# Kernel tuning notes

Hardware: AMD Instinct MI355X
Metric: run time of the kernel (lower is better)

The kernel has to match this reference:

```python
import jax, jax.numpy as jnp
import numpy as np

V, D, H, P = 50000, 128, 256, 50      # vocab, embed_dim, hidden, pos_dim
N, T = 2048, 50                        # total sentences, max words per sentence
NDOC, L = 64, 32                       # docs, sentences per doc (N = NDOC*L)
PDOC, PSENT = 50, 100                  # pos embedding table sizes


def _gru(x, Wi, Wh, bi, bh):
    """PyTorch-style GRU, batch_first. x: [B,T,Din] -> [B,T,H]."""
    B = x.shape[0]
    Hh = Wh.shape[1]
    xg = jnp.einsum('btd,gd->btg', x, Wi) + bi  # [B,T,3H] precomputed input gates

    def step(h, xg_t):
        hg = h @ Wh.T + bh
        xr, xz, xn = jnp.split(xg_t, 3, axis=-1)
        hr, hz, hn = jnp.split(hg, 3, axis=-1)
        r = jax.nn.sigmoid(xr + hr)
        z = jax.nn.sigmoid(xz + hz)
        n = jnp.tanh(xn + r * hn)
        hnew = (1.0 - z) * n + z * h
        return hnew, hnew

    h0 = jnp.zeros((B, Hh), x.dtype)
    _, hs = jax.lax.scan(step, h0, jnp.swapaxes(xg, 0, 1))
    return jnp.swapaxes(hs, 0, 1)


def _bigru(x, pf, pb):
    hf = _gru(x, *pf)
    hb = _gru(x[:, ::-1], *pb)[:, ::-1]
    return jnp.concatenate([hf, hb], axis=-1)


def _masked_max(h, lens):
    """Ragged max-pool over time: h [B,T,C], lens [B] -> [B,C]; zeros for len==0."""
    Tt = h.shape[1]
    mask = jnp.arange(Tt)[None, :, None] < lens[:, None, None]
    m = jnp.max(jnp.where(mask, h, -jnp.inf), axis=1)
    return jnp.where(lens[:, None] > 0, m, 0.0)


def setup_inputs() -> dict:
    key = jax.random.key(0)
    ks = iter(jax.random.split(key, 64))

    def w(shape, s=0.05):
        return jax.random.normal(next(ks), shape, jnp.float32) * s

    x = jax.random.randint(next(ks), (N, T), 1, V)          # no padding tokens
    doc_lens = jnp.full((NDOC,), L, dtype=jnp.int32)
    d = {'x': x, 'doc_lens': doc_lens, 'embed': w((V, D)).at[0].set(0.0)}
    for pre, din in (('w', D), ('s', 2 * H), ('d', 2 * H)):
        for suf in ('f', 'b'):
            d[f'{pre}Wi_{suf}'] = w((3 * H, din))
            d[f'{pre}Wh_{suf}'] = w((3 * H, H))
            d[f'{pre}bi_{suf}'] = w((3 * H,))
            d[f'{pre}bh_{suf}'] = w((3 * H,))
    d['doc_pos_tab'] = w((PDOC, P))
    d['sent_pos_tab'] = w((PSENT, P))
    d['w_content'] = w((2 * H,))
    d['W_sal'] = w((2 * H, 4 * H))
    d['w_dpos'] = w((P,))
    d['w_spos'] = w((P,))
    d['sent_bias'] = w((1,))
    return d


def reference(x, doc_lens, embed,
              wWi_f, wWh_f, wbi_f, wbh_f, wWi_b, wWh_b, wbi_b, wbh_b,
              sWi_f, sWh_f, sbi_f, sbh_f, sWi_b, sWh_b, sbi_b, sbh_b,
              dWi_f, dWh_f, dbi_f, dbh_f, dWi_b, dWh_b, dbi_b, dbh_b,
              doc_pos_tab, sent_pos_tab, w_content, W_sal, w_dpos, w_spos,
              sent_bias):
    sent_lens = jnp.sum(jnp.sign(x), axis=1)                 # [N]
    e = embed[x]                                             # [N,T,D]
    hw = _bigru(e, (wWi_f, wWh_f, wbi_f, wbh_f), (wWi_b, wWh_b, wbi_b, wbh_b))
    sent_vec = _masked_max(hw, sent_lens)                    # [N,2H]

    n_docs = doc_lens.shape[0]
    Ld = sent_vec.shape[0] // n_docs
    docs = sent_vec.reshape(n_docs, Ld, -1)                  # [nd,L,2H]
    hs = _bigru(docs, (sWi_f, sWh_f, sbi_f, sbh_f), (sWi_b, sWh_b, sbi_b, sbh_b))
    doc_vec = _masked_max(hs, doc_lens)                      # [nd,2H]

    hd = _bigru(doc_vec[None], (dWi_f, dWh_f, dbi_f, dbh_f),
                (dWi_b, dWh_b, dbi_b, dbh_b))[0]             # [nd,2H]
    blog_vec = jnp.max(hd, axis=0)                           # [2H]

    context = jnp.concatenate(
        [jnp.broadcast_to(blog_vec, (n_docs, blog_vec.shape[0])), doc_vec],
        axis=-1)                                             # [nd,4H]

    content = docs @ w_content                               # [nd,L]
    salience = jnp.einsum('nld,de,ne->nl', docs, W_sal, context)

    pdoc = doc_pos_tab.shape[0]
    psent = sent_pos_tab.shape[0]
    di = (jnp.arange(n_docs) * pdoc) // n_docs               # [nd]
    safe_lens = jnp.maximum(doc_lens, 1).astype(jnp.int32)
    si = (jnp.arange(Ld, dtype=jnp.int32)[None, :] * psent) // safe_lens[:, None]
    si = jnp.minimum(si, psent - 1)                          # [nd,L]
    dscore = doc_pos_tab[di] @ w_dpos                        # [nd]
    sscore = sent_pos_tab[si] @ w_spos                       # [nd,L]

    scores = content + salience + dscore[:, None] + sscore + sent_bias[0]
    return scores.reshape(-1)                                # [N]
```

## Files before the change

### kernel.cpp

```cpp
#include <hip/hip_runtime.h>
#include <math.h>

#define HID 256
#define G3 768
#define DIM 128
#define TW 50
#define NSENT 2048
#define NDOC 64
#define LSENT 32
#define PDOC 50
#define PSENT 100
#define PDIMM 50

using i32x4 = __attribute__((ext_vector_type(4))) int;

static constexpr long OFFB_W1F = 0;
static constexpr long OFFB_W2F = 294912;
static constexpr long OFFB_W1B = 589824;
static constexpr long OFFB_W2B = 884736;

static constexpr long OFF_W4_sWi_f = 589824;
static constexpr long OFF_W4_sWi_b = 983040;
static constexpr long OFF_W4_sWh_f = 1376256;
static constexpr long OFF_W4_sWh_b = 1572864;
static constexpr long OFF_W4_dWi_f = 1769472;
static constexpr long OFF_W4_dWi_b = 2162688;
static constexpr long OFF_W4_dWh_f = 2555904;
static constexpr long OFF_W4_dWh_b = 2752512;
static constexpr long OFF_W4_salT  = 2949120;
static constexpr long OFF_LENS     = 3473408;
static constexpr long OFF_SENTVEC  = 3475456;
static constexpr long OFF_XGS      = 4524032;
static constexpr long OFF_DOCVEC   = 7669760;
static constexpr long OFF_XGD      = 7702528;
static constexpr long OFF_BLOG     = 7800832;

#define SW_Q (0.3f/127.0f)
#define SX_Q (1.0f/127.0f)

__device__ __forceinline__ float sigm(float v){ return 1.0f/(1.0f+__expf(-v)); }
__device__ __forceinline__ float tanhfast(float v){ return 1.0f - 2.0f/(1.0f+__expf(2.0f*v)); }

__device__ __forceinline__ void fma4(float& acc, const float4 a, const float4 b){
  acc = fmaf(a.x, b.x, fmaf(a.y, b.y, fmaf(a.z, b.z, fmaf(a.w, b.w, acc))));
}

__device__ __forceinline__ void quant2(float v, int& a, int& b){
  float q1 = rintf(fminf(fmaxf(v*127.0f, -127.0f), 127.0f));
  a = (int)q1;
  float resid = v - q1*(1.0f/127.0f);
  b = (int)rintf(fminf(fmaxf(resid*32512.0f, -127.0f), 127.0f));
}
__device__ __forceinline__ int pack4(int a0,int a1,int a2,int a3){
  return (a0&255) | ((a1&255)<<8) | ((a2&255)<<16) | ((a3&255)<<24);
}

__global__ __launch_bounds__(256)
void k_prep_w(const float* __restrict__ wWh_f, const float* __restrict__ wWi_f,
              const float* __restrict__ wWh_b, const float* __restrict__ wWi_b,
              signed char* __restrict__ W1f, signed char* __restrict__ W2f,
              signed char* __restrict__ W1b, signed char* __restrict__ W2b)
{
  int g = blockIdx.x*256 + threadIdx.x;
  int d = g / 294912;
  int r = g % 294912;
  int mt  = r / 6144;
  int rem = r % 6144;
  int kc  = rem >> 10;
  int l   = (rem >> 4) & 63;
  int e   = r & 15;
  int row = mt*16 + (l & 15);
  int hi  = l >> 4;
  int k   = kc*64 + ((e >> 2)*16 + hi*4 + (e & 3));
  const float* Wh = d ? wWh_b : wWh_f;
  const float* Wi = d ? wWi_b : wWi_f;
  float wv = (k < 256) ? Wh[(long)row*256 + k] : Wi[(long)row*128 + (k - 256)];
  float q1 = rintf(fminf(fmaxf(wv*(1.0f/SW_Q), -127.0f), 127.0f));
  float resid = wv - q1*SW_Q;
  float q2 = rintf(fminf(fmaxf(resid*(256.0f/SW_Q), -127.0f), 127.0f));
  signed char* W1 = d ? W1b : W1f;
  signed char* W2 = d ? W2b : W2f;
  W1[r] = (signed char)(int)q1;
  W2[r] = (signed char)(int)q2;
}

struct TD { const float* src; long dst; long cnt; int sh; int R; };
struct TT { TD t[9]; };

__global__ __launch_bounds__(256) void k_transpose(TT tt, float* __restrict__ ws, long total){
  long g = (long)blockIdx.x*256 + threadIdx.x;
  if (g >= total) return;
  int k = 0; long r = g;
  while (r >= tt.t[k].cnt) { r -= tt.t[k].cnt; ++k; }
  const float* src = tt.t[k].src;
  int sh = tt.t[k].sh; int R = tt.t[k].R;
  long j = r >> sh;
  int col = (int)(r & ((1L<<sh)-1));
  ws[tt.t[k].dst + (((long)(col>>2))*R + j)*4 + (col&3)] = src[r];
}

__global__ __launch_bounds__(256) void k_lens(const int* __restrict__ x, int* __restrict__ lens){
  int n = blockIdx.x*256 + threadIdx.x;
  if (n >= NSENT) return;
  int c = 0;
  for (int t = 0; t < TW; ++t) c += (x[n*TW + t] != 0) ? 1 : 0;
  lens[n] = c;
}

__global__ __launch_bounds__(512, 2)
void k_word_i8(const int* __restrict__ x, const float* __restrict__ embed,
               const signed char* __restrict__ W1f, const signed char* __restrict__ W2f,
               const signed char* __restrict__ W1b, const signed char* __restrict__ W2b,
               const float* __restrict__ bi_f, const float* __restrict__ bi_b,
               const float* __restrict__ bh_f, const float* __restrict__ bh_b,
               const int* __restrict__ lens, float* __restrict__ sent_vec)
{
  __shared__ __align__(16) signed char X1[6*1024];
  __shared__ __align__(16) signed char X2[6*1024];
  const int blk = blockIdx.x;
  const int dir = blk & 1;
  const int n0  = (blk >> 1) * 16;
  const int tid = threadIdx.x;
  const int w    = tid >> 6;
  const int lane = tid & 63;
  const int hi4  = lane >> 4;
  const int s    = lane & 15;
  const signed char* W1 = dir ? W1b : W1f;
  const signed char* W2 = dir ? W2b : W2f;
  const float* bi = dir ? bi_b : bi_f;
  const float* bh = dir ? bh_b : bh_f;

  float b_r[2][4], b_z[2][4], b_nx[2][4], b_nh[2][4];
  #pragma unroll
  for (int q = 0; q < 2; ++q)
    #pragma unroll
    for (int i = 0; i < 4; ++i) {
      int j = (2*w + q)*16 + hi4*4 + i;
      b_r[q][i]  = bi[j]     + bh[j];
      b_z[q][i]  = bi[j+256] + bh[j+256];
      b_nx[q][i] = bi[j+512];
      b_nh[q][i] = bh[j+512];
    }
  float hold[2][4] = {{0.f,0.f,0.f,0.f},{0.f,0.f,0.f,0.f}};
  float rmax[2][4];
  #pragma unroll
  for (int q = 0; q < 2; ++q)
    #pragma unroll
    for (int i = 0; i < 4; ++i) rmax[q][i] = -INFINITY;
  const int len_s = lens[n0 + s];

  for (int i2 = tid; i2 < 1024; i2 += 512) { ((int*)X1)[i2] = 0; ((int*)X2)[i2] = 0; }

  {
    const int tx = dir ? (TW-1) : 0;
    const int s2 = tid >> 5;
    const int d0 = (tid & 31) * 4;
    const int tok = x[(n0 + s2)*TW + tx];
    const float4 ev = *(const float4*)(embed + (long)tok*DIM + d0);
    int a0,a1,a2,a3,c0,c1v,c2v,c3;
    quant2(ev.x,a0,c0); quant2(ev.y,a1,c1v); quant2(ev.z,a2,c2v); quant2(ev.w,a3,c3);
    const int kc = 4 + (d0 >> 6);
    const int kk = d0 & 63;
    const int ee0 = (kk >> 4) << 2;
    const int lp  = ((kk >> 2) & 3)*16 + s2;
    const int off = kc*1024 + lp*16 + ee0;
    *(int*)(X1 + off) = pack4(a0,a1,a2,a3);
    *(int*)(X2 + off) = pack4(c0,c1v,c2v,c3);
  }
  __syncthreads();

  for (int t = 0; t < TW; ++t) {
    i32x4 p1r[2], p23r[2], p1z[2], p23z[2], p1nh[2], p23nh[2], p1nx[2], p23nx[2];
    #pragma unroll
    for (int q = 0; q < 2; ++q) {
      p1r[q] = i32x4{0,0,0,0};  p23r[q] = i32x4{0,0,0,0};
      p1z[q] = i32x4{0,0,0,0};  p23z[q] = i32x4{0,0,0,0};
      p1nh[q]= i32x4{0,0,0,0};  p23nh[q]= i32x4{0,0,0,0};
      p1nx[q]= i32x4{0,0,0,0};  p23nx[q]= i32x4{0,0,0,0};
    }
    #pragma unroll
    for (int kc = 0; kc < 4; ++kc) {
      const i32x4 x1v = *(const i32x4*)(X1 + kc*1024 + lane*16);
      const i32x4 x2v = *(const i32x4*)(X2 + kc*1024 + lane*16);
      #pragma unroll
      for (int q = 0; q < 2; ++q) {
        const int mtr = 2*w + q;
        {
          const long fo = ((long)(mtr*6 + kc))*1024 + lane*16;
          const i32x4 a1 = *(const i32x4*)(W1 + fo);
          const i32x4 a2 = *(const i32x4*)(W2 + fo);
          p1r[q]  = __builtin_amdgcn_mfma_i32_16x16x64_i8(a1, x1v, p1r[q], 0,0,0);
          p23r[q] = __builtin_amdgcn_mfma_i32_16x16x64_i8(a1, x2v, p23r[q],0,0,0);
          p23r[q] = __builtin_amdgcn_mfma_i32_16x16x64_i8(a2, x1v, p23r[q],0,0,0);
        }
        {
          const long fo = ((long)((mtr+16)*6 + kc))*1024 + lane*16;
          const i32x4 a1 = *(const i32x4*)(W1 + fo);
          const i32x4 a2 = *(const i32x4*)(W2 + fo);
          p1z[q]  = __builtin_amdgcn_mfma_i32_16x16x64_i8(a1, x1v, p1z[q], 0,0,0);
          p23z[q] = __builtin_amdgcn_mfma_i32_16x16x64_i8(a1, x2v, p23z[q],0,0,0);
          p23z[q] = __builtin_amdgcn_mfma_i32_16x16x64_i8(a2, x1v, p23z[q],0,0,0);
        }
        {
          const long fo = ((long)((mtr+32)*6 + kc))*1024 + lane*16;
          const i32x4 a1 = *(const i32x4*)(W1 + fo);
          const i32x4 a2 = *(const i32x4*)(W2 + fo);
          p1nh[q]  = __builtin_amdgcn_mfma_i32_16x16x64_i8(a1, x1v, p1nh[q], 0,0,0);
          p23nh[q] = __builtin_amdgcn_mfma_i32_16x16x64_i8(a1, x2v, p23nh[q],0,0,0);
          p23nh[q] = __builtin_amdgcn_mfma_i32_16x16x64_i8(a2, x1v, p23nh[q],0,0,0);
        }
      }
    }
    #pragma unroll
    for (int kc = 4; kc < 6; ++kc) {
      const i32x4 x1v = *(const i32x4*)(X1 + kc*1024 + lane*16);
      const i32x4 x2v = *(const i32x4*)(X2 + kc*1024 + lane*16);
      #pragma unroll
      for (int q = 0; q < 2; ++q) {
        const int mtr = 2*w + q;
        {
          const long fo = ((long)(mtr*6 + kc))*1024 + lane*16;
          const i32x4 a1 = *(const i32x4*)(W1 + fo);
          const i32x4 a2 = *(const i32x4*)(W2 + fo);
          p1r[q]  = __builtin_amdgcn_mfma_i32_16x16x64_i8(a1, x1v, p1r[q], 0,0,0);
          p23r[q] = __builtin_amdgcn_mfma_i32_16x16x64_i8(a1, x2v, p23r[q],0,0,0);
          p23r[q] = __builtin_amdgcn_mfma_i32_16x16x64_i8(a2, x1v, p23r[q],0,0,0);
        }
        {
          const long fo = ((long)((mtr+16)*6 + kc))*1024 + lane*16;
          const i32x4 a1 = *(const i32x4*)(W1 + fo);
          const i32x4 a2 = *(const i32x4*)(W2 + fo);
          p1z[q]  = __builtin_amdgcn_mfma_i32_16x16x64_i8(a1, x1v, p1z[q], 0,0,0);
          p23z[q] = __builtin_amdgcn_mfma_i32_16x16x64_i8(a1, x2v, p23z[q],0,0,0);
          p23z[q] = __builtin_amdgcn_mfma_i32_16x16x64_i8(a2, x1v, p23z[q],0,0,0);
        }
        {
          const long fo = ((long)((mtr+32)*6 + kc))*1024 + lane*16;
          const i32x4 a1 = *(const i32x4*)(W1 + fo);
          const i32x4 a2 = *(const i32x4*)(W2 + fo);
          p1nx[q]  = __builtin_amdgcn_mfma_i32_16x16x64_i8(a1, x1v, p1nx[q], 0,0,0);
          p23nx[q] = __builtin_amdgcn_mfma_i32_16x16x64_i8(a1, x2v, p23nx[q],0,0,0);
          p23nx[q] = __builtin_amdgcn_mfma_i32_16x16x64_i8(a2, x1v, p23nx[q],0,0,0);
        }
      }
    }
    const float cc1 = SW_Q * SX_Q;
    const float cc2 = cc1 * (1.0f/256.0f);
    #pragma unroll
    for (int q = 0; q < 2; ++q)
      #pragma unroll
      for (int i = 0; i < 4; ++i) {
        float ar = fmaf(cc1, (float)p1r[q][i],  fmaf(cc2, (float)p23r[q][i],  b_r[q][i]));
        float az = fmaf(cc1, (float)p1z[q][i],  fmaf(cc2, (float)p23z[q][i],  b_z[q][i]));
        float ah = fmaf(cc1, (float)p1nh[q][i], fmaf(cc2, (float)p23nh[q][i], b_nh[q][i]));
        float ax = fmaf(cc1, (float)p1nx[q][i], fmaf(cc2, (float)p23nx[q][i], b_nx[q][i]));
        float rg = sigm(ar);
        float zg = sigm(az);
        float ng = tanhfast(ax + rg*ah);
        float hv = (1.0f - zg)*ng + zg*hold[q][i];
        hold[q][i] = hv;
        bool inm = dir ? (t >= TW - len_s) : (t < len_s);
        if (inm) rmax[q][i] = fmaxf(rmax[q][i], hv);
      }
    __syncthreads();
    #pragma unroll
    for (int q = 0; q < 2; ++q) {
      const int j0 = (2*w + q)*16 + hi4*4;
      const int kcw = j0 >> 6;
      const int kk  = j0 & 63;
      const int ee0 = (kk >> 4) << 2;
      const int lp  = ((kk >> 2) & 3)*16 + s;
      const int off = kcw*1024 + lp*16 + ee0;
      int a0,a1,a2,a3,c0,c1v,c2v,c3;
      quant2(hold[q][0],a0,c0); quant2(hold[q][1],a1,c1v);
      quant2(hold[q][2],a2,c2v); quant2(hold[q][3],a3,c3);
      *(int*)(X1 + off) = pack4(a0,a1,a2,a3);
      *(int*)(X2 + off) = pack4(c0,c1v,c2v,c3);
    }
    if (t < TW-1) {
      const int tx = dir ? (TW-2-t) : (t+1);
      const int s2 = tid >> 5;
      const int d0 = (tid & 31) * 4;
      const int tok = x[(n0 + s2)*TW + tx];
      const float4 ev = *(const float4*)(embed + (long)tok*DIM + d0);
      int a0,a1,a2,a3,c0,c1v,c2v,c3;
      quant2(ev.x,a0,c0); quant2(ev.y,a1,c1v); quant2(ev.z,a2,c2v); quant2(ev.w,a3,c3);
      const int kc = 4 + (d0 >> 6);
      const int kk = d0 & 63;
      const int ee0 = (kk >> 4) << 2;
      const int lp  = ((kk >> 2) & 3)*16 + s2;
      const int off = kc*1024 + lp*16 + ee0;
      *(int*)(X1 + off) = pack4(a0,a1,a2,a3);
      *(int*)(X2 + off) = pack4(c0,c1v,c2v,c3);
    }
    __syncthreads();
  }
  #pragma unroll
  for (int q = 0; q < 2; ++q)
    #pragma unroll
    for (int i = 0; i < 4; ++i) {
      int j = (2*w + q)*16 + hi4*4 + i;
      float v = (len_s > 0) ? rmax[q][i] : 0.0f;
      sent_vec[(long)(n0+s)*(2*HID) + dir*HID + j] = v;
    }
}

__global__ __launch_bounds__(256)
void k_gates(const float* __restrict__ A,
             const float* __restrict__ W4f, const float* __restrict__ W4b,
             const float* __restrict__ bif, const float* __restrict__ bib,
             float* __restrict__ out)
{
  __shared__ __align__(16) float a_lds[8][512];
  const int r0 = blockIdx.x * 8;
  const int j  = threadIdx.x;
  #pragma unroll
  for (int q = 0; q < 4; ++q) {
    int fi = j + q*256;
    int rr = fi >> 7; int cc = (fi & 127) * 4;
    *(float4*)(&a_lds[rr][cc]) = *(const float4*)(A + (long)(r0+rr)*512 + cc);
  }
  __syncthreads();
  float acc[6][8];
  {
    float bias[6] = { bif[j], bif[j+256], bif[j+512], bib[j], bib[j+256], bib[j+512] };
    #pragma unroll
    for (int k = 0; k < 6; ++k)
// ... 8 lines not shown
    float4 w4v= *(const float4*)(W4b + ((long)d4*G3 + j + 256)*4);
    float4 w5 = *(const float4*)(W4b + ((long)d4*G3 + j + 512)*4);
    #pragma unroll
    for (int rr = 0; rr < 8; ++rr){
      const float4 a4 = *(const float4*)(&a_lds[rr][d4*4]);
      fma4(acc[0][rr], w0, a4);
      fma4(acc[1][rr], w1, a4);
      fma4(acc[2][rr], w2, a4);
      fma4(acc[3][rr], w3, a4);
      fma4(acc[4][rr], w4v, a4);
      fma4(acc[5][rr], w5, a4);
    }
  }
  #pragma unroll
  for (int rr = 0; rr < 8; ++rr){
    long base = (long)(r0+rr)*1536;
    out[base + j      ] = acc[0][rr];
    out[base + j + 256] = acc[1][rr];
    out[base + j + 512] = acc[2][rr];
    out[base + j + 768] = acc[3][rr];
    out[base + j +1024] = acc[4][rr];
    out[base + j +1280] = acc[5][rr];
  }
}

__global__ __launch_bounds__(256)
void k_sent(const float* __restrict__ xg,
            const float* __restrict__ W4h_f, const float* __restrict__ W4h_b,
            const float* __restrict__ bh_f, const float* __restrict__ bh_b,
            const int* __restrict__ dlens, float* __restrict__ doc_vec)
{
  __shared__ __align__(16) float h_lds[2][HID];
  const int blk = blockIdx.x;
  const int dir = blk & 1;
  const int d0  = (blk >> 1) * 2;
  const int j   = threadIdx.x;
  const float* W4h = dir ? W4h_b : W4h_f;
  const float* bh  = dir ? bh_b  : bh_f;
  const float bhr = bh[j], bhz = bh[j+256], bhn = bh[j+512];
  const int lenA = dlens[d0], lenB = dlens[d0+1];
  h_lds[0][j] = 0.0f; h_lds[1][j] = 0.0f;
  float rmaxA = -INFINITY, rmaxB = -INFINITY;
  __syncthreads();
  for (int t = 0; t < LSENT; ++t) {
    const int row = dir ? (LSENT-1-t) : t;
    const float* xga = xg + ((long)(d0*LSENT + row))*1536 + dir*768;
    const float* xgb = xg + ((long)((d0+1)*LSENT + row))*1536 + dir*768;
    const float xrA = xga[j], xzA = xga[j+256], xnA = xga[j+512];
    const float xrB = xgb[j], xzB = xgb[j+256], xnB = xgb[j+512];
    float arA=bhr, azA=bhz, anA=bhn, arB=bhr, azB=bhz, anB=bhn;
    for (int d4 = 0; d4 < HID/4; ++d4) {
      const float4 wr = *(const float4*)(W4h + ((long)d4*G3 + j      )*4);
      const float4 wz = *(const float4*)(W4h + ((long)d4*G3 + j + 256)*4);
      const float4 wn = *(const float4*)(W4h + ((long)d4*G3 + j + 512)*4);
      const float4 hA = *(const float4*)(&h_lds[0][d4*4]);
      const float4 hB = *(const float4*)(&h_lds[1][d4*4]);
      fma4(arA, wr, hA); fma4(azA, wz, hA); fma4(anA, wn, hA);
      fma4(arB, wr, hB); fma4(azB, wz, hB); fma4(anB, wn, hB);
    }
    float rA = sigm(xrA + arA), zA = sigm(xzA + azA);
    float nA = tanhfast(xnA + rA*anA);
    float hAn = (1.0f - zA)*nA + zA*h_lds[0][j];
    float rB = sigm(xrB + arB), zB = sigm(xzB + azB);
    float nB = tanhfast(xnB + rB*anB);
    float hBn = (1.0f - zB)*nB + zB*h_lds[1][j];
    bool mA = dir ? (t >= LSENT - lenA) : (t < lenA);
    bool mB = dir ? (t >= LSENT - lenB) : (t < lenB);
    if (mA) rmaxA = fmaxf(rmaxA, hAn);
    if (mB) rmaxB = fmaxf(rmaxB, hBn);
    __syncthreads();
    h_lds[0][j] = hAn; h_lds[1][j] = hBn;
    __syncthreads();
  }
  doc_vec[(long)d0*512 + dir*256 + j]     = (lenA > 0) ? rmaxA : 0.0f;
  doc_vec[(long)(d0+1)*512 + dir*256 + j] = (lenB > 0) ? rmaxB : 0.0f;
}

__global__ __launch_bounds__(256)
void k_doc(const float* __restrict__ xg,
           const float* __restrict__ W4h_f, const float* __restrict__ W4h_b,
           const float* __restrict__ bh_f, const float* __restrict__ bh_b,
           float* __restrict__ blog)
{
  __shared__ __align__(16) float h_lds[HID];
  const int dir = blockIdx.x;
  const int j = threadIdx.x;
  const float* W4h = dir ? W4h_b : W4h_f;
  const float* bh  = dir ? bh_b  : bh_f;
  const float bhr = bh[j], bhz = bh[j+256], bhn = bh[j+512];
  h_lds[j] = 0.0f;
  float rmax = -INFINITY;
  __syncthreads();
  for (int t = 0; t < NDOC; ++t) {
    const int row = dir ? (NDOC-1-t) : t;
    const float* xgr = xg + (long)row*1536 + dir*768;
    const float xr = xgr[j], xz = xgr[j+256], xn = xgr[j+512];
    float ar=bhr, az=bhz, an=bhn;
    for (int d4 = 0; d4 < HID/4; ++d4) {
      const float4 wr = *(const float4*)(W4h + ((long)d4*G3 + j      )*4);
      const float4 wz = *(const float4*)(W4h + ((long)d4*G3 + j + 256)*4);
      const float4 wn = *(const float4*)(W4h + ((long)d4*G3 + j + 512)*4);
      const float4 h4 = *(const float4*)(&h_lds[d4*4]);
      fma4(ar, wr, h4); fma4(az, wz, h4); fma4(an, wn, h4);
    }
    float rg = sigm(xr + ar), zg = sigm(xz + az);
    float ng = tanhfast(xn + rg*an);
    float hn = (1.0f - zg)*ng + zg*h_lds[j];
    rmax = fmaxf(rmax, hn);
    __syncthreads();
    h_lds[j] = hn;
    __syncthreads();
  }
  blog[dir*256 + j] = rmax;
}

__global__ __launch_bounds__(256)
void k_score(const float* __restrict__ docs , const float* __restrict__ doc_vec,
             const float* __restrict__ blog, const float* __restrict__ W4sal,
             const float* __restrict__ w_content, const float* __restrict__ w_dpos,
             const float* __restrict__ w_spos, const float* __restrict__ doc_pos_tab,
             const float* __restrict__ sent_pos_tab, const float* __restrict__ sent_bias,
             const int* __restrict__ dlens, float* __restrict__ out)
{
  __shared__ __align__(16) float ctx[1024];
  __shared__ __align__(16) float cw[1024];
  const int n = blockIdx.x;
  const int j = threadIdx.x;
  ctx[j]       = blog[j];
  ctx[256 + j] = blog[256 + j];
  ctx[512 + j] = doc_vec[(long)n*512 + j];
  ctx[768 + j] = doc_vec[(long)n*512 + 256 + j];
  cw[512 + j]  = w_content[j];
  cw[768 + j]  = w_content[256 + j];
  __syncthreads();
  float acc0 = 0.0f, acc1 = 0.0f;
  for (int e4 = 0; e4 < 256; ++e4) {
// ... 55 lines not shown
  const float* sbh_f = (const float*)d_in[14];
  const float* sWi_b = (const float*)d_in[15];
  const float* sWh_b = (const float*)d_in[16];
  const float* sbi_b = (const float*)d_in[17];
  const float* sbh_b = (const float*)d_in[18];
  const float* dWi_f = (const float*)d_in[19];
  const float* dWh_f = (const float*)d_in[20];
  const float* dbi_f = (const float*)d_in[21];
  const float* dbh_f = (const float*)d_in[22];
  const float* dWi_b = (const float*)d_in[23];
  const float* dWh_b = (const float*)d_in[24];
  const float* dbi_b = (const float*)d_in[25];
  const float* dbh_b = (const float*)d_in[26];
  const float* doc_pos_tab  = (const float*)d_in[27];
  const float* sent_pos_tab = (const float*)d_in[28];
  const float* w_content    = (const float*)d_in[29];
  const float* W_sal        = (const float*)d_in[30];
  const float* w_dpos       = (const float*)d_in[31];
  const float* w_spos       = (const float*)d_in[32];
  const float* sent_bias    = (const float*)d_in[33];

  float* ws = (float*)d_ws;
  signed char* wsb = (signed char*)d_ws;
  signed char* W1f = wsb + OFFB_W1F;
  signed char* W2f = wsb + OFFB_W2F;
  signed char* W1b = wsb + OFFB_W1B;
  signed char* W2b = wsb + OFFB_W2B;

  k_prep_w<<<2304, 256, 0, stream>>>(wWh_f, wWi_f, wWh_b, wWi_b, W1f, W2f, W1b, W2b);

  TT tt;
  int idx = 0;
  auto add = [&](const float* src, long dst, int R, int Dk, int sh){
    tt.t[idx].src = src; tt.t[idx].dst = dst; tt.t[idx].cnt = (long)R*Dk;
    tt.t[idx].sh = sh; tt.t[idx].R = R; ++idx;
  };
  add(sWi_f, OFF_W4_sWi_f, 768, 512, 9);
  add(sWi_b, OFF_W4_sWi_b, 768, 512, 9);
  add(sWh_f, OFF_W4_sWh_f, 768, 256, 8);
  add(sWh_b, OFF_W4_sWh_b, 768, 256, 8);
  add(dWi_f, OFF_W4_dWi_f, 768, 512, 9);
  add(dWi_b, OFF_W4_dWi_b, 768, 512, 9);
  add(dWh_f, OFF_W4_dWh_f, 768, 256, 8);
  add(dWh_b, OFF_W4_dWh_b, 768, 256, 8);
  add(W_sal, OFF_W4_salT,  512, 1024, 10);
  long total = 0;
  for (int i = 0; i < 9; ++i) total += tt.t[i].cnt;

  k_transpose<<<(int)((total + 255)/256), 256, 0, stream>>>(tt, ws, total);
  k_lens<<<NSENT/256, 256, 0, stream>>>(x, (int*)(ws + OFF_LENS));

  k_word_i8<<<256, 512, 0, stream>>>(x, embed, W1f, W2f, W1b, W2b,
      wbi_f, wbi_b, wbh_f, wbh_b,
      (const int*)(ws + OFF_LENS), ws + OFF_SENTVEC);

  k_gates<<<NSENT/8, 256, 0, stream>>>(ws + OFF_SENTVEC,
      ws + OFF_W4_sWi_f, ws + OFF_W4_sWi_b, sbi_f, sbi_b, ws + OFF_XGS);

  k_sent<<<NDOC, 256, 0, stream>>>(ws + OFF_XGS,
      ws + OFF_W4_sWh_f, ws + OFF_W4_sWh_b, sbh_f, sbh_b,
      doc_lens, ws + OFF_DOCVEC);

  k_gates<<<NDOC/8, 256, 0, stream>>>(ws + OFF_DOCVEC,
      ws + OFF_W4_dWi_f, ws + OFF_W4_dWi_b, dbi_f, dbi_b, ws + OFF_XGD);

  k_doc<<<2, 256, 0, stream>>>(ws + OFF_XGD,
      ws + OFF_W4_dWh_f, ws + OFF_W4_dWh_b, dbh_f, dbh_b, ws + OFF_BLOG);

  k_score<<<NDOC, 256, 0, stream>>>(ws + OFF_SENTVEC, ws + OFF_DOCVEC, ws + OFF_BLOG,
      ws + OFF_W4_salT, w_content, w_dpos, w_spos,
      doc_pos_tab, sent_pos_tab, sent_bias, doc_lens, (float*)d_out);
}
```

Before: 1.880 ms.

## Move sentence and doc GRU recurrences to int8 MFMA and widen word kernel

Replaces the fp32 scalar-FMA sentence-level and document-level GRU recurrent kernels with int8 MFMA versions. These use the same two-level quantized weight split (W1 plus a residual W2) that the word GRU already uses, with weights prepared by a generalized prep kernel. The word GRU kernel now uses 1024 threads so each wave owns one 16-row gate tile instead of two, which halves per-thread serial work per timestep. The aim is to cut the latency of the long serial recurrences, at the cost of extra quantization error in the hidden-to-hidden matmuls. The doc kernel runs one batch of 16 lanes for a single sequence, so most of its MFMA work is wasted.

```diff
diff --git a/kernel.cpp b/kernel.cpp
--- a/kernel.cpp
+++ b/kernel.cpp
@@ -14,26 +14,30 @@
 
 using i32x4 = __attribute__((ext_vector_type(4))) int;
 
-static constexpr long OFFB_W1F = 0;
-static constexpr long OFFB_W2F = 294912;
-static constexpr long OFFB_W1B = 589824;
-static constexpr long OFFB_W2B = 884736;
-
-static constexpr long OFF_W4_sWi_f = 589824;
-static constexpr long OFF_W4_sWi_b = 983040;
-static constexpr long OFF_W4_sWh_f = 1376256;
-static constexpr long OFF_W4_sWh_b = 1572864;
-static constexpr long OFF_W4_dWi_f = 1769472;
-static constexpr long OFF_W4_dWi_b = 2162688;
-static constexpr long OFF_W4_dWh_f = 2555904;
-static constexpr long OFF_W4_dWh_b = 2752512;
-static constexpr long OFF_W4_salT  = 2949120;
-static constexpr long OFF_LENS     = 3473408;
-static constexpr long OFF_SENTVEC  = 3475456;
-static constexpr long OFF_XGS      = 4524032;
-static constexpr long OFF_DOCVEC   = 7669760;
-static constexpr long OFF_XGD      = 7702528;
-static constexpr long OFF_BLOG     = 7800832;
+static constexpr long OFFB_W1F  = 0;
+static constexpr long OFFB_W2F  = 294912;
+static constexpr long OFFB_W1B  = 589824;
+static constexpr long OFFB_W2B  = 884736;
+static constexpr long OFFB_SW1F = 1179648;
+static constexpr long OFFB_SW2F = 1376256;
+static constexpr long OFFB_SW1B = 1572864;
+static constexpr long OFFB_SW2B = 1769472;
+static constexpr long OFFB_DW1F = 1966080;
+static constexpr long OFFB_DW2F = 2162688;
+static constexpr long OFFB_DW1B = 2359296;
+static constexpr long OFFB_DW2B = 2555904;
+
+static constexpr long OFF_W4_sWi_f = 688128;
+static constexpr long OFF_W4_sWi_b = 1081344;
+static constexpr long OFF_W4_dWi_f = 1474560;
+static constexpr long OFF_W4_dWi_b = 1867776;
+static constexpr long OFF_W4_salT  = 2260992;
+static constexpr long OFF_LENS     = 2785280;
+static constexpr long OFF_SENTVEC  = 2787328;
+static constexpr long OFF_XGS      = 3835904;
+static constexpr long OFF_DOCVEC   = 6981632;
+static constexpr long OFF_XGD      = 7014400;
+static constexpr long OFF_BLOG     = 7112704;
 
 #define SW_Q (0.3f/127.0f)
 #define SX_Q (1.0f/127.0f)
@@ -55,37 +59,43 @@
   return (a0&255) | ((a1&255)<<8) | ((a2&255)<<16) | ((a3&255)<<24);
 }
 
-__global__ __launch_bounds__(256)
-void k_prep_w(const float* __restrict__ wWh_f, const float* __restrict__ wWi_f,
-              const float* __restrict__ wWh_b, const float* __restrict__ wWi_b,
-              signed char* __restrict__ W1f, signed char* __restrict__ W2f,
-              signed char* __restrict__ W1b, signed char* __restrict__ W2b)
-{
-  int g = blockIdx.x*256 + threadIdx.x;
-  int d = g / 294912;
-  int r = g % 294912;
-  int mt  = r / 6144;
-  int rem = r % 6144;
+__device__ __forceinline__ void mfma3(const signed char* __restrict__ W1,
+                                      const signed char* __restrict__ W2, long fo,
+                                      i32x4 x1v, i32x4 x2v, i32x4& p1, i32x4& p23){
+  const i32x4 a1 = *(const i32x4*)(W1 + fo);
+  const i32x4 a2 = *(const i32x4*)(W2 + fo);
+  p1  = __builtin_amdgcn_mfma_i32_16x16x64_i8(a1, x1v, p1, 0,0,0);
+  p23 = __builtin_amdgcn_mfma_i32_16x16x64_i8(a1, x2v, p23,0,0,0);
+  p23 = __builtin_amdgcn_mfma_i32_16x16x64_i8(a2, x1v, p23,0,0,0);
+}
+
+struct PE { const float* Wh; const float* Wi; signed char* d1; signed char* d2; long cnt; int nkc; };
+struct PP { PE e[6]; };
+__global__ __launch_bounds__(256) void k_prep(PP pp, long total){
+  long g = (long)blockIdx.x*256 + threadIdx.x;
+  if (g >= total) return;
+  int k = 0; long r = g;
+  while (r >= pp.e[k].cnt) { r -= pp.e[k].cnt; ++k; }
+  const float* Wh = pp.e[k].Wh;
+  const float* Wi = pp.e[k].Wi;
+  int span = pp.e[k].nkc << 10;
+  int mt  = (int)(r / span);
+  int rem = (int)(r % span);
   int kc  = rem >> 10;
   int l   = (rem >> 4) & 63;
-  int e   = r & 15;
+  int e16 = rem & 15;
   int row = mt*16 + (l & 15);
-  int hi  = l >> 4;
-  int k   = kc*64 + ((e >> 2)*16 + hi*4 + (e & 3));
-  const float* Wh = d ? wWh_b : wWh_f;
-  const float* Wi = d ? wWi_b : wWi_f;
-  float wv = (k < 256) ? Wh[(long)row*256 + k] : Wi[(long)row*128 + (k - 256)];
+  int kk  = kc*64 + ((e16>>2)*16 + (l>>4)*4 + (e16&3));
+  float wv = (kk < 256) ? Wh[(long)row*256 + kk] : Wi[(long)row*128 + (kk-256)];
   float q1 = rintf(fminf(fmaxf(wv*(1.0f/SW_Q), -127.0f), 127.0f));
   float resid = wv - q1*SW_Q;
   float q2 = rintf(fminf(fmaxf(resid*(256.0f/SW_Q), -127.0f), 127.0f));
-  signed char* W1 = d ? W1b : W1f;
-  signed char* W2 = d ? W2b : W2f;
-  W1[r] = (signed char)(int)q1;
-  W2[r] = (signed char)(int)q2;
+  pp.e[k].d1[r] = (signed char)(int)q1;
+  pp.e[k].d2[r] = (signed char)(int)q2;
 }
 
 struct TD { const float* src; long dst; long cnt; int sh; int R; };
-struct TT { TD t[9]; };
+struct TT { TD t[5]; };
 
 __global__ __launch_bounds__(256) void k_transpose(TT tt, float* __restrict__ ws, long total){
   long g = (long)blockIdx.x*256 + threadIdx.x;
@@ -107,7 +117,7 @@
   lens[n] = c;
 }
 
-__global__ __launch_bounds__(512, 2)
+__global__ __launch_bounds__(1024, 4)
 void k_word_i8(const int* __restrict__ x, const float* __restrict__ embed,
                const signed char* __restrict__ W1f, const signed char* __restrict__ W2f,
                const signed char* __restrict__ W1b, const signed char* __restrict__ W2b,
@@ -125,33 +135,28 @@
   const int lane = tid & 63;
   const int hi4  = lane >> 4;
   const int s    = lane & 15;
+  const int j0   = w*16 + hi4*4;
   const signed char* W1 = dir ? W1b : W1f;
   const signed char* W2 = dir ? W2b : W2f;
   const float* bi = dir ? bi_b : bi_f;
   const float* bh = dir ? bh_b : bh_f;
 
-  float b_r[2][4], b_z[2][4], b_nx[2][4], b_nh[2][4];
-  #pragma unroll
-  for (int q = 0; q < 2; ++q)
-    #pragma unroll
-    for (int i = 0; i < 4; ++i) {
-      int j = (2*w + q)*16 + hi4*4 + i;
-      b_r[q][i]  = bi[j]     + bh[j];
-      b_z[q][i]  = bi[j+256] + bh[j+256];
-      b_nx[q][i] = bi[j+512];
-      b_nh[q][i] = bh[j+512];
-    }
-  float hold[2][4] = {{0.f,0.f,0.f,0.f},{0.f,0.f,0.f,0.f}};
-  float rmax[2][4];
-  #pragma unroll
-  for (int q = 0; q < 2; ++q)
-    #pragma unroll
-    for (int i = 0; i < 4; ++i) rmax[q][i] = -INFINITY;
+  float b_r[4], b_z[4], b_nx[4], b_nh[4];
+  #pragma unroll
+  for (int i = 0; i < 4; ++i) {
+    int j = j0 + i;
+    b_r[i]  = bi[j]     + bh[j];
+    b_z[i]  = bi[j+256] + bh[j+256];
+    b_nx[i] = bi[j+512];
+    b_nh[i] = bh[j+512];
+  }
+  float hold[4] = {0.f,0.f,0.f,0.f};
+  float rmax[4] = {-INFINITY,-INFINITY,-INFINITY,-INFINITY};
   const int len_s = lens[n0 + s];
 
-  for (int i2 = tid; i2 < 1024; i2 += 512) { ((int*)X1)[i2] = 0; ((int*)X2)[i2] = 0; }
-
-  {
+  for (int i2 = tid; i2 < 1536; i2 += 1024) { ((int*)X1)[i2] = 0; ((int*)X2)[i2] = 0; }
+
+  if (tid < 512) {
     const int tx = dir ? (TW-1) : 0;
     const int s2 = tid >> 5;
     const int d0 = (tid & 31) * 4;
@@ -170,114 +175,49 @@
   __syncthreads();
 
   for (int t = 0; t < TW; ++t) {
-    i32x4 p1r[2], p23r[2], p1z[2], p23z[2], p1nh[2], p23nh[2], p1nx[2], p23nx[2];
-    #pragma unroll
-    for (int q = 0; q < 2; ++q) {
-      p1r[q] = i32x4{0,0,0,0};  p23r[q] = i32x4{0,0,0,0};
-      p1z[q] = i32x4{0,0,0,0};  p23z[q] = i32x4{0,0,0,0};
-      p1nh[q]= i32x4{0,0,0,0};  p23nh[q]= i32x4{0,0,0,0};
-      p1nx[q]= i32x4{0,0,0,0};  p23nx[q]= i32x4{0,0,0,0};
-    }
-    #pragma unroll
-    for (int kc = 0; kc < 4; ++kc) {
+    i32x4 p1r  = {0,0,0,0}, p23r  = {0,0,0,0};
+    i32x4 p1z  = {0,0,0,0}, p23z  = {0,0,0,0};
+    i32x4 p1nh = {0,0,0,0}, p23nh = {0,0,0,0};
+    i32x4 p1nx = {0,0,0,0}, p23nx = {0,0,0,0};
+    #pragma unroll
+    for (int kc = 0; kc < 6; ++kc) {
       const i32x4 x1v = *(const i32x4*)(X1 + kc*1024 + lane*16);
       const i32x4 x2v = *(const i32x4*)(X2 + kc*1024 + lane*16);
-      #pragma unroll
-      for (int q = 0; q < 2; ++q) {
-        const int mtr = 2*w + q;
-        {
-          const long fo = ((long)(mtr*6 + kc))*1024 + lane*16;
-          const i32x4 a1 = *(const i32x4*)(W1 + fo);
-          const i32x4 a2 = *(const i32x4*)(W2 + fo);
-          p1r[q]  = __builtin_amdgcn_mfma_i32_16x16x64_i8(a1, x1v, p1r[q], 0,0,0);
-          p23r[q] = __builtin_amdgcn_mfma_i32_16x16x64_i8(a1, x2v, p23r[q],0,0,0);
-          p23r[q] = __builtin_amdgcn_mfma_i32_16x16x64_i8(a2, x1v, p23r[q],0,0,0);
-        }
-        {
-          const long fo = ((long)((mtr+16)*6 + kc))*1024 + lane*16;
-          const i32x4 a1 = *(const i32x4*)(W1 + fo);
-          const i32x4 a2 = *(const i32x4*)(W2 + fo);
-          p1z[q]  = __builtin_amdgcn_mfma_i32_16x16x64_i8(a1, x1v, p1z[q], 0,0,0);
-          p23z[q] = __builtin_amdgcn_mfma_i32_16x16x64_i8(a1, x2v, p23z[q],0,0,0);
-          p23z[q] = __builtin_amdgcn_mfma_i32_16x16x64_i8(a2, x1v, p23z[q],0,0,0);
-        }
-        {
-          const long fo = ((long)((mtr+32)*6 + kc))*1024 + lane*16;
-          const i32x4 a1 = *(const i32x4*)(W1 + fo);
-          const i32x4 a2 = *(const i32x4*)(W2 + fo);
-          p1nh[q]  = __builtin_amdgcn_mfma_i32_16x16x64_i8(a1, x1v, p1nh[q], 0,0,0);
-          p23nh[q] = __builtin_amdgcn_mfma_i32_16x16x64_i8(a1, x2v, p23nh[q],0,0,0);
-          p23nh[q] = __builtin_amdgcn_mfma_i32_16x16x64_i8(a2, x1v, p23nh[q],0,0,0);
-        }
-      }
-    }
-    #pragma unroll
-    for (int kc = 4; kc < 6; ++kc) {
-      const i32x4 x1v = *(const i32x4*)(X1 + kc*1024 + lane*16);
-      const i32x4 x2v = *(const i32x4*)(X2 + kc*1024 + lane*16);
-      #pragma unroll
-      for (int q = 0; q < 2; ++q) {
-        const int mtr = 2*w + q;
-        {
-          const long fo = ((long)(mtr*6 + kc))*1024 + lane*16;
-          const i32x4 a1 = *(const i32x4*)(W1 + fo);
-          const i32x4 a2 = *(const i32x4*)(W2 + fo);
-          p1r[q]  = __builtin_amdgcn_mfma_i32_16x16x64_i8(a1, x1v, p1r[q], 0,0,0);
-          p23r[q] = __builtin_amdgcn_mfma_i32_16x16x64_i8(a1, x2v, p23r[q],0,0,0);
-          p23r[q] = __builtin_amdgcn_mfma_i32_16x16x64_i8(a2, x1v, p23r[q],0,0,0);
-        }
-        {
-          const long fo = ((long)((mtr+16)*6 + kc))*1024 + lane*16;
-          const i32x4 a1 = *(const i32x4*)(W1 + fo);
-          const i32x4 a2 = *(const i32x4*)(W2 + fo);
-          p1z[q]  = __builtin_amdgcn_mfma_i32_16x16x64_i8(a1, x1v, p1z[q], 0,0,0);
-          p23z[q] = __builtin_amdgcn_mfma_i32_16x16x64_i8(a1, x2v, p23z[q],0,0,0);
-          p23z[q] = __builtin_amdgcn_mfma_i32_16x16x64_i8(a2, x1v, p23z[q],0,0,0);
-        }
-        {
-          const long fo = ((long)((mtr+32)*6 + kc))*1024 + lane*16;
-          const i32x4 a1 = *(const i32x4*)(W1 + fo);
-          const i32x4 a2 = *(const i32x4*)(W2 + fo);
-          p1nx[q]  = __builtin_amdgcn_mfma_i32_16x16x64_i8(a1, x1v, p1nx[q], 0,0,0);
-          p23nx[q] = __builtin_amdgcn_mfma_i32_16x16x64_i8(a1, x2v, p23nx[q],0,0,0);
-          p23nx[q] = __builtin_amdgcn_mfma_i32_16x16x64_i8(a2, x1v, p23nx[q],0,0,0);
-        }
-      }
+      mfma3(W1, W2, ((long)(w*6      + kc))*1024 + lane*16, x1v, x2v, p1r, p23r);
+      mfma3(W1, W2, ((long)((w+16)*6 + kc))*1024 + lane*16, x1v, x2v, p1z, p23z);
+      if (kc < 4) mfma3(W1, W2, ((long)((w+32)*6 + kc))*1024 + lane*16, x1v, x2v, p1nh, p23nh);
+      else        mfma3(W1, W2, ((long)((w+32)*6 + kc))*1024 + lane*16, x1v, x2v, p1nx, p23nx);
     }
     const float cc1 = SW_Q * SX_Q;
     const float cc2 = cc1 * (1.0f/256.0f);
     #pragma unroll
-    for (int q = 0; q < 2; ++q)
-      #pragma unroll
-      for (int i = 0; i < 4; ++i) {
-        float ar = fmaf(cc1, (float)p1r[q][i],  fmaf(cc2, (float)p23r[q][i],  b_r[q][i]));
-        float az = fmaf(cc1, (float)p1z[q][i],  fmaf(cc2, (float)p23z[q][i],  b_z[q][i]));
-        float ah = fmaf(cc1, (float)p1nh[q][i], fmaf(cc2, (float)p23nh[q][i], b_nh[q][i]));
-        float ax = fmaf(cc1, (float)p1nx[q][i], fmaf(cc2, (float)p23nx[q][i], b_nx[q][i]));
-        float rg = sigm(ar);
-        float zg = sigm(az);
-        float ng = tanhfast(ax + rg*ah);
-        float hv = (1.0f - zg)*ng + zg*hold[q][i];
-        hold[q][i] = hv;
-        bool inm = dir ? (t >= TW - len_s) : (t < len_s);
-        if (inm) rmax[q][i] = fmaxf(rmax[q][i], hv);
-      }
+    for (int i = 0; i < 4; ++i) {
+      float ar = fmaf(cc1, (float)p1r[i],  fmaf(cc2, (float)p23r[i],  b_r[i]));
+      float az = fmaf(cc1, (float)p1z[i],  fmaf(cc2, (float)p23z[i],  b_z[i]));
+      float ah = fmaf(cc1, (float)p1nh[i], fmaf(cc2, (float)p23nh[i], b_nh[i]));
+      float ax = fmaf(cc1, (float)p1nx[i], fmaf(cc2, (float)p23nx[i], b_nx[i]));
+      float rg = sigm(ar);
+      float zg = sigm(az);
+      float ng = tanhfast(ax + rg*ah);
+      float hv = (1.0f - zg)*ng + zg*hold[i];
+      hold[i] = hv;
+      bool inm = dir ? (t >= TW - len_s) : (t < len_s);
+      if (inm) rmax[i] = fmaxf(rmax[i], hv);
+    }
     __syncthreads();
-    #pragma unroll
-    for (int q = 0; q < 2; ++q) {
-      const int j0 = (2*w + q)*16 + hi4*4;
+    {
       const int kcw = j0 >> 6;
       const int kk  = j0 & 63;
       const int ee0 = (kk >> 4) << 2;
       const int lp  = ((kk >> 2) & 3)*16 + s;
       const int off = kcw*1024 + lp*16 + ee0;
       int a0,a1,a2,a3,c0,c1v,c2v,c3;
-      quant2(hold[q][0],a0,c0); quant2(hold[q][1],a1,c1v);
-      quant2(hold[q][2],a2,c2v); quant2(hold[q][3],a3,c3);
+      quant2(hold[0],a0,c0); quant2(hold[1],a1,c1v);
+      quant2(hold[2],a2,c2v); quant2(hold[3],a3,c3);
       *(int*)(X1 + off) = pack4(a0,a1,a2,a3);
       *(int*)(X2 + off) = pack4(c0,c1v,c2v,c3);
     }
-    if (t < TW-1) {
+    if (t < TW-1 && tid < 512) {
       const int tx = dir ? (TW-2-t) : (t+1);
       const int s2 = tid >> 5;
       const int d0 = (tid & 31) * 4;
@@ -296,13 +236,186 @@
     __syncthreads();
   }
   #pragma unroll
-  for (int q = 0; q < 2; ++q)
+  for (int i = 0; i < 4; ++i) {
+    float v = (len_s > 0) ? rmax[i] : 0.0f;
+    sent_vec[(long)(n0+s)*(2*HID) + dir*HID + j0 + i] = v;
+  }
+}
+
+__global__ __launch_bounds__(1024, 4)
+void k_sent_i8(const float* __restrict__ xg,
+               const signed char* __restrict__ SW1f, const signed char* __restrict__ SW2f,
+               const signed char* __restrict__ SW1b, const signed char* __restrict__ SW2b,
+               const float* __restrict__ bh_f, const float* __restrict__ bh_b,
+               const int* __restrict__ dlens, float* __restrict__ doc_vec)
+{
+  __shared__ __align__(16) signed char X1[4*1024];
+  __shared__ __align__(16) signed char X2[4*1024];
+  const int blk = blockIdx.x;
+  const int dir = blk & 1;
+  const int g   = blk >> 1;
+  const int tid = threadIdx.x;
+  const int w    = tid >> 6;
+  const int lane = tid & 63;
+  const int hi4  = lane >> 4;
+  const int s    = lane & 15;
+  const int j0   = w*16 + hi4*4;
+  const int d    = g*16 + s;
+  const signed char* W1 = dir ? SW1b : SW1f;
+  const signed char* W2 = dir ? SW2b : SW2f;
+  const float* bh = dir ? bh_b : bh_f;
+  float b_r[4], b_z[4], b_nh[4];
+  #pragma unroll
+  for (int i = 0; i < 4; ++i) {
+    b_r[i]  = bh[j0+i];
+    b_z[i]  = bh[j0+i+256];
+    b_nh[i] = bh[j0+i+512];
+  }
+  float hold[4] = {0.f,0.f,0.f,0.f};
+  float rmax[4] = {-INFINITY,-INFINITY,-INFINITY,-INFINITY};
+  const int len_d = dlens[d];
+  ((int*)X1)[tid] = 0; ((int*)X2)[tid] = 0;
+  __syncthreads();
+
+  for (int t = 0; t < LSENT; ++t) {
+    const int row = dir ? (LSENT-1-t) : t;
+    const float* xgr = xg + ((long)(d*LSENT + row))*1536 + dir*768;
+    const float4 xr4 = *(const float4*)(xgr + j0);
+    const float4 xz4 = *(const float4*)(xgr + 256 + j0);
+    const float4 xn4 = *(const float4*)(xgr + 512 + j0);
+    const float xr[4] = {xr4.x, xr4.y, xr4.z, xr4.w};
+    const float xz[4] = {xz4.x, xz4.y, xz4.z, xz4.w};
+    const float xn[4] = {xn4.x, xn4.y, xn4.z, xn4.w};
+    i32x4 p1r = {0,0,0,0}, p23r = {0,0,0,0};
+    i32x4 p1z = {0,0,0,0}, p23z = {0,0,0,0};
+    i32x4 p1n = {0,0,0,0}, p23n = {0,0,0,0};
+    #pragma unroll
+    for (int kc = 0; kc < 4; ++kc) {
+      const i32x4 x1v = *(const i32x4*)(X1 + kc*1024 + lane*16);
+      const i32x4 x2v = *(const i32x4*)(X2 + kc*1024 + lane*16);
+      mfma3(W1, W2, ((long)(w*4      + kc))*1024 + lane*16, x1v, x2v, p1r, p23r);
+      mfma3(W1, W2, ((long)((w+16)*4 + kc))*1024 + lane*16, x1v, x2v, p1z, p23z);
+      mfma3(W1, W2, ((long)((w+32)*4 + kc))*1024 + lane*16, x1v, x2v, p1n, p23n);
+    }
+    const float cc1 = SW_Q * SX_Q;
+    const float cc2 = cc1 * (1.0f/256.0f);
     #pragma unroll
     for (int i = 0; i < 4; ++i) {
-      int j = (2*w + q)*16 + hi4*4 + i;
-      float v = (len_s > 0) ? rmax[q][i] : 0.0f;
-      sent_vec[(long)(n0+s)*(2*HID) + dir*HID + j] = v;
-    }
+      float ar = xr[i] + fmaf(cc1, (float)p1r[i], fmaf(cc2, (float)p23r[i], b_r[i]));
+      float az = xz[i] + fmaf(cc1, (float)p1z[i], fmaf(cc2, (float)p23z[i], b_z[i]));
+      float ah =         fmaf(cc1, (float)p1n[i], fmaf(cc2, (float)p23n[i], b_nh[i]));
+      float rg = sigm(ar);
+      float zg = sigm(az);
+      float ng = tanhfast(xn[i] + rg*ah);
+      float hv = (1.0f - zg)*ng + zg*hold[i];
+      hold[i] = hv;
+      bool inm = dir ? (t >= LSENT - len_d) : (t < len_d);
+      if (inm) rmax[i] = fmaxf(rmax[i], hv);
+    }
+    __syncthreads();
+    {
+      const int kcw = j0 >> 6;
+      const int kk  = j0 & 63;
+      const int ee0 = (kk >> 4) << 2;
+      const int lp  = ((kk >> 2) & 3)*16 + s;
+      const int off = kcw*1024 + lp*16 + ee0;
+      int a0,a1,a2,a3,c0,c1v,c2v,c3;
+      quant2(hold[0],a0,c0); quant2(hold[1],a1,c1v);
+      quant2(hold[2],a2,c2v); quant2(hold[3],a3,c3);
+      *(int*)(X1 + off) = pack4(a0,a1,a2,a3);
+      *(int*)(X2 + off) = pack4(c0,c1v,c2v,c3);
+    }
+    __syncthreads();
+  }
+  #pragma unroll
+  for (int i = 0; i < 4; ++i)
+    doc_vec[(long)d*512 + dir*256 + j0 + i] = (len_d > 0) ? rmax[i] : 0.0f;
+}
+
+__global__ __launch_bounds__(1024, 4)
+void k_doc_i8(const float* __restrict__ xg,
+              const signed char* __restrict__ DW1f, const signed char* __restrict__ DW2f,
+              const signed char* __restrict__ DW1b, const signed char* __restrict__ DW2b,
+              const float* __restrict__ bh_f, const float* __restrict__ bh_b,
+              float* __restrict__ blog)
+{
+  __shared__ __align__(16) signed char X1[4*1024];
+  __shared__ __align__(16) signed char X2[4*1024];
+  const int dir = blockIdx.x;
+  const int tid = threadIdx.x;
+  const int w    = tid >> 6;
+  const int lane = tid & 63;
+  const int hi4  = lane >> 4;
+  const int s    = lane & 15;
+  const int j0   = w*16 + hi4*4;
+  const signed char* W1 = dir ? DW1b : DW1f;
+  const signed char* W2 = dir ? DW2b : DW2f;
+  const float* bh = dir ? bh_b : bh_f;
+  float b_r[4], b_z[4], b_nh[4];
+  #pragma unroll
+  for (int i = 0; i < 4; ++i) {
+    b_r[i]  = bh[j0+i];
+    b_z[i]  = bh[j0+i+256];
+    b_nh[i] = bh[j0+i+512];
+  }
+  float hold[4] = {0.f,0.f,0.f,0.f};
+  float rmax[4] = {-INFINITY,-INFINITY,-INFINITY,-INFINITY};
+  ((int*)X1)[tid] = 0; ((int*)X2)[tid] = 0;
+  __syncthreads();
+
+  for (int t = 0; t < NDOC; ++t) {
+    const int row = dir ? (NDOC-1-t) : t;
+    const float* xgr = xg + (long)row*1536 + dir*768;
+    const float4 xr4 = *(const float4*)(xgr + j0);
+    const float4 xz4 = *(const float4*)(xgr + 256 + j0);
+    const float4 xn4 = *(const float4*)(xgr + 512 + j0);
+    const float xr[4] = {xr4.x, xr4.y, xr4.z, xr4.w};
+    const float xz[4] = {xz4.x, xz4.y, xz4.z, xz4.w};
+    const float xn[4] = {xn4.x, xn4.y, xn4.z, xn4.w};
+    i32x4 p1r = {0,0,0,0}, p23r = {0,0,0,0};
+    i32x4 p1z = {0,0,0,0}, p23z = {0,0,0,0};
+    i32x4 p1n = {0,0,0,0}, p23n = {0,0,0,0};
+    #pragma unroll
+    for (int kc = 0; kc < 4; ++kc) {
+      const i32x4 x1v = *(const i32x4*)(X1 + kc*1024 + lane*16);
+      const i32x4 x2v = *(const i32x4*)(X2 + kc*1024 + lane*16);
+      mfma3(W1, W2, ((long)(w*4      + kc))*1024 + lane*16, x1v, x2v, p1r, p23r);
+      mfma3(W1, W2, ((long)((w+16)*4 + kc))*1024 + lane*16, x1v, x2v, p1z, p23z);
+      mfma3(W1, W2, ((long)((w+32)*4 + kc))*1024 + lane*16, x1v, x2v, p1n, p23n);
+    }
+    const float cc1 = SW_Q * SX_Q;
+    const float cc2 = cc1 * (1.0f/256.0f);
+    #pragma unroll
+    for (int i = 0; i < 4; ++i) {
+      float ar = xr[i] + fmaf(cc1, (float)p1r[i], fmaf(cc2, (float)p23r[i], b_r[i]));
+      float az = xz[i] + fmaf(cc1, (float)p1z[i], fmaf(cc2, (float)p23z[i], b_z[i]));
+      float ah =         fmaf(cc1, (float)p1n[i], fmaf(cc2, (float)p23n[i], b_nh[i]));
+      float rg = sigm(ar);
+      float zg = sigm(az);
+      float ng = tanhfast(xn[i] + rg*ah);
+      float hv = (1.0f - zg)*ng + zg*hold[i];
+      hold[i] = hv;
+      rmax[i] = fmaxf(rmax[i], hv);
+    }
+    __syncthreads();
+    if (s == 0) {
+      const int kcw = j0 >> 6;
+      const int kk  = j0 & 63;
+      const int ee0 = (kk >> 4) << 2;
+      const int lp  = ((kk >> 2) & 3)*16;
+      const int off = kcw*1024 + lp*16 + ee0;
+      int a0,a1,a2,a3,c0,c1v,c2v,c3;
+      quant2(hold[0],a0,c0); quant2(hold[1],a1,c1v);
+      quant2(hold[2],a2,c2v); quant2(hold[3],a3,c3);
+      *(int*)(X1 + off) = pack4(a0,a1,a2,a3);
+      *(int*)(X2 + off) = pack4(c0,c1v,c2v,c3);
+    }
+    __syncthreads();
+  }
+  if (s == 0) {
+    #pragma unroll
+    for (int i = 0; i < 4; ++i) blog[dir*256 + j0 + i] = rmax[i];
+  }
 }
 
 __global__ __launch_bounds__(256)
@@ -357,96 +470,6 @@
     out[base + j +1024] = acc[4][rr];
     out[base + j +1280] = acc[5][rr];
   }
-}
-
-__global__ __launch_bounds__(256)
-void k_sent(const float* __restrict__ xg,
-            const float* __restrict__ W4h_f, const float* __restrict__ W4h_b,
-            const float* __restrict__ bh_f, const float* __restrict__ bh_b,
-            const int* __restrict__ dlens, float* __restrict__ doc_vec)
-{
-  __shared__ __align__(16) float h_lds[2][HID];
-  const int blk = blockIdx.x;
-  const int dir = blk & 1;
-  const int d0  = (blk >> 1) * 2;
-  const int j   = threadIdx.x;
-  const float* W4h = dir ? W4h_b : W4h_f;
-  const float* bh  = dir ? bh_b  : bh_f;
-  const float bhr = bh[j], bhz = bh[j+256], bhn = bh[j+512];
-  const int lenA = dlens[d0], lenB = dlens[d0+1];
-  h_lds[0][j] = 0.0f; h_lds[1][j] = 0.0f;
-  float rmaxA = -INFINITY, rmaxB = -INFINITY;
-  __syncthreads();
-  for (int t = 0; t < LSENT; ++t) {
-    const int row = dir ? (LSENT-1-t) : t;
-    const float* xga = xg + ((long)(d0*LSENT + row))*1536 + dir*768;
-    const float* xgb = xg + ((long)((d0+1)*LSENT + row))*1536 + dir*768;
-    const float xrA = xga[j], xzA = xga[j+256], xnA = xga[j+512];
-    const float xrB = xgb[j], xzB = xgb[j+256], xnB = xgb[j+512];
-    float arA=bhr, azA=bhz, anA=bhn, arB=bhr, azB=bhz, anB=bhn;
-    for (int d4 = 0; d4 < HID/4; ++d4) {
-      const float4 wr = *(const float4*)(W4h + ((long)d4*G3 + j      )*4);
-      const float4 wz = *(const float4*)(W4h + ((long)d4*G3 + j + 256)*4);
-      const float4 wn = *(const float4*)(W4h + ((long)d4*G3 + j + 512)*4);
-      const float4 hA = *(const float4*)(&h_lds[0][d4*4]);
-      const float4 hB = *(const float4*)(&h_lds[1][d4*4]);
-      fma4(arA, wr, hA); fma4(azA, wz, hA); fma4(anA, wn, hA);
-      fma4(arB, wr, hB); fma4(azB, wz, hB); fma4(anB, wn, hB);
-    }
-    float rA = sigm(xrA + arA), zA = sigm(xzA + azA);
-    float nA = tanhfast(xnA + rA*anA);
-    float hAn = (1.0f - zA)*nA + zA*h_lds[0][j];
-    float rB = sigm(xrB + arB), zB = sigm(xzB + azB);
-    float nB = tanhfast(xnB + rB*anB);
-    float hBn = (1.0f - zB)*nB + zB*h_lds[1][j];
-    bool mA = dir ? (t >= LSENT - lenA) : (t < lenA);
-    bool mB = dir ? (t >= LSENT - lenB) : (t < lenB);
-    if (mA) rmaxA = fmaxf(rmaxA, hAn);
-    if (mB) rmaxB = fmaxf(rmaxB, hBn);
-    __syncthreads();
-    h_lds[0][j] = hAn; h_lds[1][j] = hBn;
-    __syncthreads();
-  }
-  doc_vec[(long)d0*512 + dir*256 + j]     = (lenA > 0) ? rmaxA : 0.0f;
-  doc_vec[(long)(d0+1)*512 + dir*256 + j] = (lenB > 0) ? rmaxB : 0.0f;
-}
-
-__global__ __launch_bounds__(256)
-void k_doc(const float* __restrict__ xg,
-           const float* __restrict__ W4h_f, const float* __restrict__ W4h_b,
-           const float* __restrict__ bh_f, const float* __restrict__ bh_b,
-           float* __restrict__ blog)
-{
-  __shared__ __align__(16) float h_lds[HID];
-  const int dir = blockIdx.x;
-  const int j = threadIdx.x;
-  const float* W4h = dir ? W4h_b : W4h_f;
-  const float* bh  = dir ? bh_b  : bh_f;
-  const float bhr = bh[j], bhz = bh[j+256], bhn = bh[j+512];
-  h_lds[j] = 0.0f;
-  float rmax = -INFINITY;
-  __syncthreads();
-  for (int t = 0; t < NDOC; ++t) {
-    const int row = dir ? (NDOC-1-t) : t;
-    const float* xgr = xg + (long)row*1536 + dir*768;
-    const float xr = xgr[j], xz = xgr[j+256], xn = xgr[j+512];
-    float ar=bhr, az=bhz, an=bhn;
-    for (int d4 = 0; d4 < HID/4; ++d4) {
-      const float4 wr = *(const float4*)(W4h + ((long)d4*G3 + j      )*4);
-      const float4 wz = *(const float4*)(W4h + ((long)d4*G3 + j + 256)*4);
-      const float4 wn = *(const float4*)(W4h + ((long)d4*G3 + j + 512)*4);
-      const float4 h4 = *(const float4*)(&h_lds[d4*4]);
-      fma4(ar, wr, h4); fma4(az, wz, h4); fma4(an, wn, h4);
-    }
-    float rg = sigm(xr + ar), zg = sigm(xz + az);
-    float ng = tanhfast(xn + rg*an);
-    float hn = (1.0f - zg)*ng + zg*h_lds[j];
-    rmax = fmaxf(rmax, hn);
-    __syncthreads();
-    h_lds[j] = hn;
-    __syncthreads();
-  }
-  blog[dir*256 + j] = rmax;
 }
 
 __global__ __launch_bounds__(256)
@@ -548,12 +571,20 @@
 
   float* ws = (float*)d_ws;
   signed char* wsb = (signed char*)d_ws;
-  signed char* W1f = wsb + OFFB_W1F;
-  signed char* W2f = wsb + OFFB_W2F;
-  signed char* W1b = wsb + OFFB_W1B;
-  signed char* W2b = wsb + OFFB_W2B;
-
-  k_prep_w<<<2304, 256, 0, stream>>>(wWh_f, wWi_f, wWh_b, wWi_b, W1f, W2f, W1b, W2b);
+
+  PP pp;
+  auto setp = [&](int i, const float* Wh, const float* Wi, long d1, long d2, long cnt, int nkc){
+    pp.e[i].Wh = Wh; pp.e[i].Wi = Wi; pp.e[i].d1 = wsb + d1; pp.e[i].d2 = wsb + d2;
+    pp.e[i].cnt = cnt; pp.e[i].nkc = nkc;
+  };
+  setp(0, wWh_f, wWi_f, OFFB_W1F,  OFFB_W2F,  294912, 6);
+  setp(1, wWh_b, wWi_b, OFFB_W1B,  OFFB_W2B,  294912, 6);
+  setp(2, sWh_f, sWh_f, OFFB_SW1F, OFFB_SW2F, 196608, 4);
+  setp(3, sWh_b, sWh_b, OFFB_SW1B, OFFB_SW2B, 196608, 4);
+  setp(4, dWh_f, dWh_f, OFFB_DW1F, OFFB_DW2F, 196608, 4);
+  setp(5, dWh_b, dWh_b, OFFB_DW1B, OFFB_DW2B, 196608, 4);
+  long ptotal = 2*294912 + 4*196608;
+  k_prep<<<(int)((ptotal + 255)/256), 256, 0, stream>>>(pp, ptotal);
 
   TT tt;
   int idx = 0;
@@ -563,35 +594,32 @@
   };
   add(sWi_f, OFF_W4_sWi_f, 768, 512, 9);
   add(sWi_b, OFF_W4_sWi_b, 768, 512, 9);
-  add(sWh_f, OFF_W4_sWh_f, 768, 256, 8);
-  add(sWh_b, OFF_W4_sWh_b, 768, 256, 8);
   add(dWi_f, OFF_W4_dWi_f, 768, 512, 9);
   add(dWi_b, OFF_W4_dWi_b, 768, 512, 9);
-  add(dWh_f, OFF_W4_dWh_f, 768, 256, 8);
-  add(dWh_b, OFF_W4_dWh_b, 768, 256, 8);
   add(W_sal, OFF_W4_salT,  512, 1024, 10);
   long total = 0;
-  for (int i = 0; i < 9; ++i) total += tt.t[i].cnt;
-
+  for (int i = 0; i < 5; ++i) total += tt.t[i].cnt;
   k_transpose<<<(int)((total + 255)/256), 256, 0, stream>>>(tt, ws, total);
   k_lens<<<NSENT/256, 256, 0, stream>>>(x, (int*)(ws + OFF_LENS));
 
-  k_word_i8<<<256, 512, 0, stream>>>(x, embed, W1f, W2f, W1b, W2b,
+  k_word_i8<<<256, 1024, 0, stream>>>(x, embed,
+      wsb + OFFB_W1F, wsb + OFFB_W2F, wsb + OFFB_W1B, wsb + OFFB_W2B,
       wbi_f, wbi_b, wbh_f, wbh_b,
       (const int*)(ws + OFF_LENS), ws + OFF_SENTVEC);
 
   k_gates<<<NSENT/8, 256, 0, stream>>>(ws + OFF_SENTVEC,
       ws + OFF_W4_sWi_f, ws + OFF_W4_sWi_b, sbi_f, sbi_b, ws + OFF_XGS);
 
-  k_sent<<<NDOC, 256, 0, stream>>>(ws + OFF_XGS,
-      ws + OFF_W4_sWh_f, ws + OFF_W4_sWh_b, sbh_f, sbh_b,
-      doc_lens, ws + OFF_DOCVEC);
+  k_sent_i8<<<8, 1024, 0, stream>>>(ws + OFF_XGS,
+      wsb + OFFB_SW1F, wsb + OFFB_SW2F, wsb + OFFB_SW1B, wsb + OFFB_SW2B,
+      sbh_f, sbh_b, doc_lens, ws + OFF_DOCVEC);
 
   k_gates<<<NDOC/8, 256, 0, stream>>>(ws + OFF_DOCVEC,
       ws + OFF_W4_dWi_f, ws + OFF_W4_dWi_b, dbi_f, dbi_b, ws + OFF_XGD);
 
-  k_doc<<<2, 256, 0, stream>>>(ws + OFF_XGD,
-      ws + OFF_W4_dWh_f, ws + OFF_W4_dWh_b, dbh_f, dbh_b, ws + OFF_BLOG);
+  k_doc_i8<<<2, 1024, 0, stream>>>(ws + OFF_XGD,
+      wsb + OFFB_DW1F, wsb + OFFB_DW2F, wsb + OFFB_DW1B, wsb + OFFB_DW2B,
+      dbh_f, dbh_b, ws + OFF_BLOG);
 
   k_score<<<NDOC, 256, 0, stream>>>(ws + OFF_SENTVEC, ws + OFF_DOCVEC, ws + OFF_BLOG,
       ws + OFF_W4_salT, w_content, w_dpos, w_spos,
```

Result: faster. 1.753 ms (-6.8%).
